# Optimization experiments

Measured on AMD Instinct MI355X. Metric: run time of the kernel, lower is better.

## Reference

```python
import jax, jax.numpy as jnp
import numpy as np

H = 16  # n_heads from init_kwargs


def setup_inputs() -> dict:
    key = jax.random.key(0)
    ks = jax.random.split(key, 9)
    B, N, D = 4, 4096, 1024
    mk = lambda k, shape: jax.random.normal(k, shape, dtype=jnp.float32) * 0.02
    return {
        "x": jax.random.normal(ks[0], (B, N, D), dtype=jnp.float32),
        "Wq": mk(ks[1], (D, D)), "bq": mk(ks[2], (D,)),
        "Wk": mk(ks[3], (D, D)), "bk": mk(ks[4], (D,)),
        "Wv": mk(ks[5], (D, D)), "bv": mk(ks[6], (D,)),
        "Wo": mk(ks[7], (D, D)), "bo": mk(ks[8], (D,)),
    }


def _split_heads(t):
    B, N, D = t.shape
    return t.reshape(B, N, H, D // H).transpose(0, 2, 1, 3)  # b h n d


def reference(x, Wq, bq, Wk, bk, Wv, bv, Wo, bo):
    B, N, D = x.shape
    d_head = D // H
    s = (d_head ** 0.5) ** (-0.25)
    q = _split_heads(x @ Wq + bq)
    # NOTE: original computes key(x) but immediately overwrites it with
    # q.softmax(dim=-2); key projection is dead code. We replicate exactly.
    _ = x @ Wk + bk  # dead, kept for parameter-shape parity
    v = _split_heads(x @ Wv + bv)
    q = jax.nn.softmax(q, axis=-1) * s            # softmax over d_head
    k = jax.nn.softmax(q, axis=-2) * s            # softmax of q over seq dim (faithful!)
    ctx = jnp.einsum('bhnd,bhne->bhde', k, v)     # k^T @ v, [B,H,d,d]
    attn = jnp.einsum('bhnd,bhde->bhne', q, ctx)  # q @ ctx, [B,H,N,d]
    attn = attn.transpose(0, 2, 1, 3).reshape(B, N, D)
    # n_heads > 1 -> to_out linear; dropout is identity in eval mode
    return attn @ Wo + bo
```

## Files before the change

kernel.cpp:

```cpp
#include <hip/hip_runtime.h>

typedef unsigned short u16;
typedef __attribute__((ext_vector_type(8))) short short8;
typedef __attribute__((ext_vector_type(4))) float f4;
typedef __attribute__((ext_vector_type(8))) unsigned short us8;

__device__ __forceinline__ u16 f2bf(float f) {
    unsigned u = __float_as_uint(f);
    u += 0x7FFFu + ((u >> 16) & 1u);
    return (u16)(u >> 16);
}
__device__ __forceinline__ float bf2f(u16 h) {
    return __uint_as_float(((unsigned)h) << 16);
}

#define GLD16(gp, lp) __builtin_amdgcn_global_load_lds( \
    (const __attribute__((address_space(1))) void*)(gp), \
    (__attribute__((address_space(3))) void*)(lp), 16, 0, 0)

#define SCALE_S 0.594603557501360533f

__global__ __launch_bounds__(256) void convert_f32_bf16(const float* __restrict__ in,
                                                        u16* __restrict__ out) {
    const size_t i = (size_t)blockIdx.x * 256 + threadIdx.x;
    const float4* p = (const float4*)in + i * 2;
    float4 a = p[0], b = p[1];
    us8 r;
    r[0] = f2bf(a.x); r[1] = f2bf(a.y); r[2] = f2bf(a.z); r[3] = f2bf(a.w);
    r[4] = f2bf(b.x); r[5] = f2bf(b.y); r[6] = f2bf(b.z); r[7] = f2bf(b.w);
    *(us8*)(out + i * 8) = r;
}

__global__ __launch_bounds__(256) void transpose_convert3(
    const float* __restrict__ Wq, const float* __restrict__ Wv, const float* __restrict__ Wo,
    u16* __restrict__ WqvT, u16* __restrict__ WoT) {
    const float* W; u16* out;
    if (blockIdx.z == 0)      { W = Wq; out = WqvT; }
    else if (blockIdx.z == 1) { W = Wv; out = WqvT + 1024 * 1024; }
    else                      { W = Wo; out = WoT; }
    __shared__ float tile[32][33];
    const int tx = threadIdx.x, ty = threadIdx.y;
    const int x = blockIdx.x * 32 + tx;
#pragma unroll
    for (int i = 0; i < 4; ++i) {
        const int y = blockIdx.y * 32 + ty + i * 8;
        tile[ty + i * 8][tx] = W[(size_t)y * 1024 + x];
    }
    __syncthreads();
#pragma unroll
    for (int i = 0; i < 4; ++i) {
        const int yo = blockIdx.x * 32 + ty + i * 8;
        const int xo = blockIdx.y * 32 + tx;
        out[(size_t)yo * 1024 + xo] = f2bf(tile[tx][ty + i * 8]);
    }
}

__global__ void concat_bias(const float* __restrict__ bq, const float* __restrict__ bv,
                            float* __restrict__ bqv) {
    const int i = blockIdx.x * 256 + threadIdx.x;
    bqv[i] = (i < 1024) ? bq[i] : bv[i - 1024];
}

#define BAR8() do { asm volatile("" ::: "memory"); __builtin_amdgcn_s_barrier(); \
                    asm volatile("" ::: "memory"); } while (0)
#define WAITV(n) asm volatile("s_waitcnt vmcnt(" #n ")" ::: "memory")

#define STG2(arr, p, half) do { \
    const u16* s_ = (p) + (size_t)(half) * 128 * 1024; \
    u16* d_ = &arr[half][ldst]; \
    GLD16(s_, d_); \
    GLD16(s_ + (size_t)64 * 1024, d_ + 64 * 64); \
} while (0)

#define MFMA_CL(base) \
    _Pragma("unroll") for (int kk_ = 0; kk_ < 2; ++kk_) \
    _Pragma("unroll") for (int i_ = 0; i_ < 4; ++i_) \
    _Pragma("unroll") for (int j_ = 0; j_ < 4; ++j_) \
        acc[(base) + i_][j_] = __builtin_amdgcn_mfma_f32_16x16x32_bf16( \
            bf[j_][kk_], af[i_][kk_], acc[(base) + i_][j_], 0, 0, 0);

#define KTILE3(AsR, BsR, AsW, BsW) do { \
    short8 bf[4][2]; \
    _Pragma("unroll") for (int j_ = 0; j_ < 4; ++j_) \
    _Pragma("unroll") for (int kk_ = 0; kk_ < 2; ++kk_) \
        bf[j_][kk_] = *(const short8*)&BsR[bhalf][(brow + j_ * 16 + lrow) * 64 + (kg0 ^ (kk_ << 5))]; \
    { \
        short8 af[4][2]; \
        _Pragma("unroll") for (int i_ = 0; i_ < 4; ++i_) \
        _Pragma("unroll") for (int kk_ = 0; kk_ < 2; ++kk_) \
            af[i_][kk_] = *(const short8*)&AsR[wrow][(i_ * 16 + lrow) * 64 + (kg0 ^ (kk_ << 5))]; \
        STG2(AsW, aP, 0); STG2(AsW, aP, 1); aP += 64; \
        __builtin_amdgcn_s_setprio(1); \
        MFMA_CL(0) \
        __builtin_amdgcn_s_setprio(0); \
    } \
    { \
        short8 af[4][2]; \
        _Pragma("unroll") for (int i_ = 0; i_ < 4; ++i_) \
        _Pragma("unroll") for (int kk_ = 0; kk_ < 2; ++kk_) \
            af[i_][kk_] = *(const short8*)&AsR[wrow][((64 + i_ * 16 + lrow)) * 64 + (kg0 ^ (kk_ << 5))]; \
        BAR8(); \
        STG2(BsW, bP, 0); STG2(BsW, bP, 1); bP += 64; \
        __builtin_amdgcn_s_setprio(1); \
        MFMA_CL(4) \
        __builtin_amdgcn_s_setprio(0); \
    } \
    WAITV(8); \
    BAR8(); \
} while (0)

#define KTILE_NOSYNC(AsR, BsR) do { \
    short8 bf[4][2]; \
    _Pragma("unroll") for (int j_ = 0; j_ < 4; ++j_) \
    _Pragma("unroll") for (int kk_ = 0; kk_ < 2; ++kk_) \
        bf[j_][kk_] = *(const short8*)&BsR[bhalf][(brow + j_ * 16 + lrow) * 64 + (kg0 ^ (kk_ << 5))]; \
    _Pragma("unroll") for (int h_ = 0; h_ < 2; ++h_) { \
        short8 af[4][2]; \
        _Pragma("unroll") for (int i_ = 0; i_ < 4; ++i_) \
        _Pragma("unroll") for (int kk_ = 0; kk_ < 2; ++kk_) \
            af[i_][kk_] = *(const short8*)&AsR[wrow][((h_ * 64 + i_ * 16 + lrow)) * 64 + (kg0 ^ (kk_ << 5))]; \
        if (h_ == 0) { MFMA_CL(0) } else { MFMA_CL(4) } \
    } \
} while (0)

#define GEMM_PRO_AND_LOOP() \
    STG2(Bs0, bS, 0); STG2(Bs0, bS, 1); \
    STG2(As0, aS, 0); STG2(As0, aS, 1); \
    { const u16* b1 = bS + 64; STG2(Bs1, b1, 0); STG2(Bs1, b1, 1); } \
    { const u16* a1 = aS + 64; STG2(As1, a1, 0); STG2(As1, a1, 1); } \
    WAITV(8); \
    BAR8(); \
    const u16* aP = aS + 128; \
    const u16* bP = bS + 128; \
    for (int it6 = 0; it6 < 2; ++it6) { \
        KTILE3(As0, Bs0, As2, Bs0); \
        KTILE3(As1, Bs1, As0, Bs1); \
        KTILE3(As2, Bs0, As1, Bs0); \
        KTILE3(As0, Bs1, As2, Bs1); \
        KTILE3(As1, Bs0, As0, Bs0); \
        KTILE3(As2, Bs1, As1, Bs1); \
    } \
    KTILE3(As0, Bs0, As2, Bs0);   \
    KTILE3(As1, Bs1, As0, Bs1);   \
    WAITV(0); \
    BAR8(); \
    KTILE_NOSYNC(As2, Bs0);       \
    KTILE_NOSYNC(As0, Bs1);

__global__ __launch_bounds__(512, 2) void gemm_qv(
    const u16* __restrict__ A, const u16* __restrict__ BT,
    const float* __restrict__ bias,
    u16* __restrict__ qsOut, u16* __restrict__ vOut)
{
    __shared__ u16 As0[2][128 * 64], As1[2][128 * 64], As2[2][128 * 64];
    __shared__ u16 Bs0[2][128 * 64], Bs1[2][128 * 64];
    const int t = threadIdx.x;
    const int l = t & 63, w = t >> 6;
    const int quad = l >> 4, lrow = l & 15;
    const int wrow = w >> 2, wcol = w & 3;
    const int bhalf = wcol >> 1, brow = (wcol & 1) * 64;

    int bx, by;
    {
        const int id = blockIdx.x + (int)gridDim.x * blockIdx.y;
        const int xcd = id & 7, j = id >> 3;
        const int xs = (int)gridDim.x >> 3;
        bx = xcd * xs + (j % xs);
        by = j / xs;
    }
    const int m0 = bx * 256, n0 = by * 256;

    const int lr0 = t >> 3;
    const int cg = ((t & 7) ^ (lr0 & 7)) * 8;
    const int ldst = lr0 * 64 + (t & 7) * 8;
    const u16* aS = A  + (size_t)(m0 + lr0) * 1024 + cg;
    const u16* bS = BT + (size_t)(n0 + lr0) * 1024 + cg;

    const int kg0 = (quad ^ (lrow & 7)) << 3;
    f4 acc[8][4] = {};

    GEMM_PRO_AND_LOOP()

    const int colh = n0 + wcol * 64;
    const bool isQ = n0 < 1024;
    float4 bs4[4];
#pragma unroll
    for (int j = 0; j < 4; ++j)
        bs4[j] = *(const float4*)&bias[colh + j * 16 + quad * 4];

#pragma unroll
    for (int i = 0; i < 8; ++i) {
        const int m = m0 + wrow * 128 + i * 16 + lrow;
        float v[4][4];
#pragma unroll
        for (int j = 0; j < 4; ++j) {
            v[j][0] = acc[i][j][0] + bs4[j].x;
            v[j][1] = acc[i][j][1] + bs4[j].y;
            v[j][2] = acc[i][j][2] + bs4[j].z;
            v[j][3] = acc[i][j][3] + bs4[j].w;
        }
        if (isQ) {
            float mx = v[0][0];
#pragma unroll
            for (int j = 0; j < 4; ++j)
#pragma unroll
                for (int r = 0; r < 4; ++r) mx = fmaxf(mx, v[j][r]);
            mx = fmaxf(mx, __shfl_xor(mx, 16));
            mx = fmaxf(mx, __shfl_xor(mx, 32));
            float sm = 0.f;
#pragma unroll
            for (int j = 0; j < 4; ++j)
#pragma unroll
                for (int r = 0; r < 4; ++r) { v[j][r] = __expf(v[j][r] - mx); sm += v[j][r]; }
            sm += __shfl_xor(sm, 16);
            sm += __shfl_xor(sm, 32);
            const float inv = SCALE_S / sm;
            u16* qp = qsOut + (size_t)m * 1024 + colh + quad * 4;
#pragma unroll
            for (int j = 0; j < 4; ++j) {
                uint2 pk;
                pk.x = (unsigned)f2bf(v[j][0] * inv) | ((unsigned)f2bf(v[j][1] * inv) << 16);
                pk.y = (unsigned)f2bf(v[j][2] * inv) | ((unsigned)f2bf(v[j][3] * inv) << 16);
                *(uint2*)(qp + j * 16) = pk;
            }
        } else {
            u16* vp = vOut + (size_t)m * 1024 + (colh - 1024) + quad * 4;
#pragma unroll
            for (int j = 0; j < 4; ++j) {
                uint2 pk;
                pk.x = (unsigned)f2bf(v[j][0]) | ((unsigned)f2bf(v[j][1]) << 16);
                pk.y = (unsigned)f2bf(v[j][2]) | ((unsigned)f2bf(v[j][3]) << 16);
                *(uint2*)(vp + j * 16) = pk;
            }
        }
    }
}

__global__ __launch_bounds__(512, 2) void gemm_out(
    const u16* __restrict__ A, const u16* __restrict__ BT,
    const float* __restrict__ bias, float* __restrict__ C)
{
    __shared__ u16 As0[2][128 * 64], As1[2][128 * 64], As2[2][128 * 64];
    __shared__ u16 Bs0[2][128 * 64], Bs1[2][128 * 64];
    const int t = threadIdx.x;
    const int l = t & 63, w = t >> 6;
    const int quad = l >> 4, lrow = l & 15;
    const int wrow = w >> 2, wcol = w & 3;
    const int bhalf = wcol >> 1, brow = (wcol & 1) * 64;
    const int z = blockIdx.z;
    A  += (size_t)z * (4096 * 1024);
    BT += (size_t)z * (1024 * 1024);
    C  += (size_t)z * (4096 * 1024);

    int bx, by;
    {
        const int id = blockIdx.x + (int)gridDim.x * blockIdx.y;
        const int xcd = id & 7, j = id >> 3;
        const int xs = (int)gridDim.x >> 3;
        bx = xcd * xs + (j % xs);
        by = j / xs;
    }
    const int m0 = bx * 256, n0 = by * 256;

    const int lr0 = t >> 3;
    const int cg = ((t & 7) ^ (lr0 & 7)) * 8;
    const int ldst = lr0 * 64 + (t & 7) * 8;
    const u16* aS = A  + (size_t)(m0 + lr0) * 1024 + cg;
    const u16* bS = BT + (size_t)(n0 + lr0) * 1024 + cg;

    const int kg0 = (quad ^ (lrow & 7)) << 3;
    f4 acc[8][4] = {};

    GEMM_PRO_AND_LOOP()

    const int colh = n0 + wcol * 64;
    float4 bs4[4];
#pragma unroll
    for (int j = 0; j < 4; ++j)
        bs4[j] = *(const float4*)&bias[colh + j * 16 + quad * 4];
#pragma unroll
    for (int i = 0; i < 8; ++i) {
        const int m = m0 + wrow * 128 + i * 16 + lrow;
        float* cp = C + (size_t)m * 1024 + colh + quad * 4;
#pragma unroll
        for (int j = 0; j < 4; ++j) {
            float4 o;
            o.x = acc[i][j][0] + bs4[j].x;
            o.y = acc[i][j][1] + bs4[j].y;
            o.z = acc[i][j][2] + bs4[j].z;
            o.w = acc[i][j][3] + bs4[j].w;
            *(float4*)(cp + j * 16) = o;
        }
    }
}

__global__ __launch_bounds__(256) void ctx_mfma(
    const u16* __restrict__ qs, const u16* __restrict__ vb,
    float* __restrict__ Mpart, float* __restrict__ Zpart)
{
    __shared__ __align__(16) u16 Et[2][64 * 64];
    __shared__ __align__(16) u16 Vt[2][64 * 64];
    const int t = threadIdx.x;
    const int w = t >> 6, l = t & 63;
    const int quad = l >> 4, lrow = l & 15;
    const int g = blockIdx.x;
    const int split = blockIdx.y;
    const int b = g >> 4, h = g & 15;

    const int n0 = (l & 31) * 2;
    const int d0 = w * 16 + (l >> 5) * 8;
    const u16* qp = qs + ((size_t)b * 4096 + (size_t)split * 256 + n0) * 1024 + h * 64 + d0;
    const u16* vp = vb + ((size_t)b * 4096 + (size_t)split * 256 + n0) * 1024 + h * 64 + d0;

    f4 acc[4] = {};
    float zacc[8] = {};

    us8 q8a = *(const us8*)qp;
    us8 q8b = *(const us8*)(qp + 1024);
    us8 v8a = *(const us8*)vp;
    us8 v8b = *(const us8*)(vp + 1024);

    for (int slab = 0; slab < 4; ++slab) {
        unsigned epk[8], vpk[8];
#pragma unroll
        for (int j = 0; j < 8; ++j) {
            float ea = __expf(bf2f((u16)q8a[j]));
            float eb = __expf(bf2f((u16)q8b[j]));
            zacc[j] += ea + eb;
            epk[j] = (unsigned)f2bf(ea) | ((unsigned)f2bf(eb) << 16);
            vpk[j] = (unsigned)(u16)v8a[j] | ((unsigned)(u16)v8b[j] << 16);
        }
        if (slab < 3) {
            qp += 64 * 1024; vp += 64 * 1024;
            q8a = *(const us8*)qp;  q8b = *(const us8*)(qp + 1024);
            v8a = *(const us8*)vp;  v8b = *(const us8*)(vp + 1024);
        }
        u16* et = Et[slab & 1];
        u16* vt = Vt[slab & 1];
#pragma unroll
        for (int j = 0; j < 8; ++j) {
            const int d = d0 + j;
            const int off = d * 64 + (((n0 >> 3) ^ (d & 7)) << 3) + (n0 & 7);
            *(unsigned*)&et[off] = epk[j];
            *(unsigned*)&vt[off] = vpk[j];
        }
        __syncthreads();
#pragma unroll
        for (int kk = 0; kk < 2; ++kk) {
            const int blk = ((kk * 4 + quad) ^ (lrow & 7)) << 3;
            short8 a = *(const short8*)&et[(w * 16 + lrow) * 64 + blk];
#pragma unroll
            for (int j = 0; j < 4; ++j) {
                short8 bfr = *(const short8*)&vt[(j * 16 + lrow) * 64 + blk];
                acc[j] = __builtin_amdgcn_mfma_f32_16x16x32_bf16(bfr, a, acc[j], 0, 0, 0);
            }
        }
    }

#pragma unroll
    for (int j = 0; j < 8; ++j) {
        zacc[j] += __shfl_xor(zacc[j], 1);
        zacc[j] += __shfl_xor(zacc[j], 2);
        zacc[j] += __shfl_xor(zacc[j], 4);
        zacc[j] += __shfl_xor(zacc[j], 8);
        zacc[j] += __shfl_xor(zacc[j], 16);
    }
    if ((l & 31) == 0) {
        float* zp = Zpart + ((size_t)split * 64 + g) * 64 + d0;
#pragma unroll
        for (int j = 0; j < 8; ++j) zp[j] = zacc[j];
    }

    float* mp = Mpart + ((size_t)split * 64 + g) * 4096;
#pragma unroll
    for (int j = 0; j < 4; ++j) {
        float4 o;
        o.x = acc[j][0]; o.y = acc[j][1]; o.z = acc[j][2]; o.w = acc[j][3];
        *(float4*)&mp[(w * 16 + lrow) * 64 + j * 16 + quad * 4] = o;
    }
}

__global__ __launch_bounds__(256) void ctx_norm(const float* __restrict__ Mpart,
                                                const float* __restrict__ Zpart,
                                                float* __restrict__ ctx2) {
    const int g = blockIdx.x >> 2, q = blockIdx.x & 3, t = threadIdx.x;
    __shared__ float rz[64];
    if (t < 64) {
        float zsum = 0.f;
#pragma unroll
        for (int s = 0; s < 16; ++s) zsum += Zpart[((size_t)s * 64 + g) * 64 + t];
        rz[t] = SCALE_S / zsum;
    }
    __syncthreads();
    const int base = q * 1024;
    for (int ii = t; ii < 1024; ii += 256) {
        const int idx = base + ii;
        float m = 0.f;
#pragma unroll
        for (int s = 0; s < 16; ++s) m += Mpart[((size_t)s * 64 + g) * 4096 + idx];
        ctx2[(size_t)g * 4096 + idx] = m * rz[idx >> 6];
    }
}

__global__ __launch_bounds__(256) void woprime(const float* __restrict__ ctx2,
                                               const u16* __restrict__ WoT,
                                               u16* __restrict__ WopT) {
    __shared__ float ctxT[64 * 65];
    __shared__ __align__(16) u16 wo[64 * 64];
    const int t = threadIdx.x;
    const int jt = blockIdx.x, h = blockIdx.y, b = blockIdx.z;
    const int g = b * 16 + h;
    for (int idx = t; idx < 4096; idx += 256) {
        const int d = idx >> 6, e = idx & 63;
        ctxT[e * 65 + d] = ctx2[(size_t)g * 4096 + idx];
    }
    const int j0 = jt * 64;
#pragma unroll
    for (int c = 0; c < 2; ++c) {
        const int ii = c * 256 + t;
        const int j = ii >> 3, c8 = ii & 7;
        *(us8*)&wo[j * 64 + c8 * 8] = *(const us8*)&WoT[(size_t)(j0 + j) * 1024 + h * 64 + c8 * 8];
    }
    __syncthreads();
    const int d = t & 63, w = t >> 6;
    float accj[16] = {};
    for (int eb = 0; eb < 8; ++eb) {
        float c8[8];
#pragma unroll
        for (int e = 0; e < 8; ++e) c8[e] = ctxT[(eb * 8 + e) * 65 + d];
#pragma unroll
        for (int jj = 0; jj < 16; ++jj) {
            us8 w8 = *(const us8*)&wo[(jj * 4 + w) * 64 + eb * 8];
#pragma unroll
            for (int e = 0; e < 8; ++e)
                accj[jj] += bf2f((u16)w8[e]) * c8[e];
        }
    }
#pragma unroll
    for (int jj = 0; jj < 16; ++jj)
        WopT[(size_t)b * 1048576 + (size_t)(j0 + jj * 4 + w) * 1024 + h * 64 + d] = f2bf(accj[jj]);
}

extern "C" void kernel_launch(void* const* d_in, const int* in_sizes, int n_in,
                              void* d_out, int out_size, void* d_ws, size_t ws_size,
                              hipStream_t stream)
{
    const float* x  = (const float*)d_in[0];
    const float* Wq = (const float*)d_in[1];
    const float* bq = (const float*)d_in[2];
    const float* Wv = (const float*)d_in[5];
    const float* bv = (const float*)d_in[6];
    const float* Wo = (const float*)d_in[7];
    const float* bo = (const float*)d_in[8];
    float* out = (float*)d_out;

    char* ws = (char*)d_ws;
    size_t o = 0;
    auto alloc = [&](size_t bytes) { char* p = ws + o; o = (o + bytes + 255) & ~(size_t)255; return p; };
    u16*   x_bf  = (u16*)  alloc(16384ull * 1024 * 2);
    u16*   WqvT  = (u16*)  alloc(2048ull * 1024 * 2);
    u16*   WoT   = (u16*)  alloc(1024ull * 1024 * 2);
    float* bqv   = (float*)alloc(2048ull * 4);
    u16*   qs    = (u16*)  alloc(16384ull * 1024 * 2);
    u16*   vbuf  = (u16*)  alloc(16384ull * 1024 * 2);
    float* Zpart = (float*)alloc(16ull * 64 * 64 * 4);
    float* ctx2  = (float*)alloc(64ull * 4096 * 4);
    u16*   WopT  = (u16*)  alloc(4ull * 1024 * 1024 * 2);
    float* Mpart = (float*)x_bf;
    (void)ws_size; (void)in_sizes; (void)n_in; (void)out_size;

    convert_f32_bf16<<<8192, 256, 0, stream>>>(x, x_bf);
    transpose_convert3<<<dim3(32, 32, 3), dim3(32, 8), 0, stream>>>(Wq, Wv, Wo, WqvT, WoT);
    concat_bias<<<8, 256, 0, stream>>>(bq, bv, bqv);

    gemm_qv<<<dim3(64, 8), 512, 0, stream>>>(x_bf, WqvT, bqv, qs, vbuf);
    ctx_mfma<<<dim3(64, 16), 256, 0, stream>>>(qs, vbuf, Mpart, Zpart);
    ctx_norm<<<256, 256, 0, stream>>>(Mpart, Zpart, ctx2);
    woprime<<<dim3(16, 16, 4), 256, 0, stream>>>(ctx2, WoT, WopT);
    gemm_out<<<dim3(16, 4, 4), 512, 0, stream>>>(qs, WopT, bo, out);
}
```

Baseline: 300.2 us.

## Prefetch next B fragments into registers across K-tiles in QV GEMM

Restructures the GEMM main loop so each K-tile reads both A-fragment halves up front and uses B fragments already held in registers (bfc) from the previous iteration. The next tile's B fragments are read from LDS mid-tile, between the two MFMA clusters, which overlaps LDS reads with compute. The vmcnt wait moves earlier and the barrier placement changes. This costs extra VGPRs for the doubled fragment buffers, which could spill or lower occupancy at launch_bounds(512,2).

Result: slower. 307.7 us (+2.5%).

```diff
diff --git a/kernel.cpp b/kernel.cpp
--- a/kernel.cpp
+++ b/kernel.cpp
@@ -72,80 +72,83 @@
     GLD16(s_ + (size_t)64 * 1024, d_ + 64 * 64); \
 } while (0)
 
-#define MFMA_CL(base) \
+#define RD_AF(af, AsR, roff) \
+    _Pragma("unroll") for (int i_ = 0; i_ < 4; ++i_) \
+    _Pragma("unroll") for (int kk_ = 0; kk_ < 2; ++kk_) \
+        af[i_][kk_] = *(const short8*)&AsR[wrow][((roff) + i_ * 16 + lrow) * 64 + (kg0 ^ (kk_ << 5))];
+
+#define RD_BF(bfa, BsX) \
+    _Pragma("unroll") for (int j_ = 0; j_ < 4; ++j_) \
+    _Pragma("unroll") for (int kk_ = 0; kk_ < 2; ++kk_) \
+        bfa[j_][kk_] = *(const short8*)&BsX[bhalf][(brow + j_ * 16 + lrow) * 64 + (kg0 ^ (kk_ << 5))];
+
+#define MFMA_C(base, bfa, afa) \
     _Pragma("unroll") for (int kk_ = 0; kk_ < 2; ++kk_) \
     _Pragma("unroll") for (int i_ = 0; i_ < 4; ++i_) \
     _Pragma("unroll") for (int j_ = 0; j_ < 4; ++j_) \
         acc[(base) + i_][j_] = __builtin_amdgcn_mfma_f32_16x16x32_bf16( \
-            bf[j_][kk_], af[i_][kk_], acc[(base) + i_][j_], 0, 0, 0);
-
-#define KTILE3(AsR, BsR, AsW, BsW) do { \
-    short8 bf[4][2]; \
+            bfa[j_][kk_], afa[i_][kk_], acc[(base) + i_][j_], 0, 0, 0);
+
+#define KTILE_D(AsR, BsN, AsW, BsW) do { \
+    short8 af0[4][2], af1[4][2]; \
+    RD_AF(af0, AsR, 0) \
+    RD_AF(af1, AsR, 64) \
+    STG2(AsW, aP, 0); STG2(AsW, aP, 1); aP += 64; \
+    WAITV(4); \
+    __builtin_amdgcn_s_setprio(1); MFMA_C(0, bfc, af0) __builtin_amdgcn_s_setprio(0); \
+    BAR8(); \
+    short8 bfn[4][2]; \
+    RD_BF(bfn, BsN) \
+    STG2(BsW, bP, 0); STG2(BsW, bP, 1); bP += 64; \
+    __builtin_amdgcn_s_setprio(1); MFMA_C(4, bfc, af1) __builtin_amdgcn_s_setprio(0); \
+    BAR8(); \
     _Pragma("unroll") for (int j_ = 0; j_ < 4; ++j_) \
     _Pragma("unroll") for (int kk_ = 0; kk_ < 2; ++kk_) \
-        bf[j_][kk_] = *(const short8*)&BsR[bhalf][(brow + j_ * 16 + lrow) * 64 + (kg0 ^ (kk_ << 5))]; \
-    { \
-        short8 af[4][2]; \
-        _Pragma("unroll") for (int i_ = 0; i_ < 4; ++i_) \
-        _Pragma("unroll") for (int kk_ = 0; kk_ < 2; ++kk_) \
-            af[i_][kk_] = *(const short8*)&AsR[wrow][(i_ * 16 + lrow) * 64 + (kg0 ^ (kk_ << 5))]; \
-        STG2(AsW, aP, 0); STG2(AsW, aP, 1); aP += 64; \
-        __builtin_amdgcn_s_setprio(1); \
-        MFMA_CL(0) \
-        __builtin_amdgcn_s_setprio(0); \
-    } \
-    { \
-        short8 af[4][2]; \
-        _Pragma("unroll") for (int i_ = 0; i_ < 4; ++i_) \
-        _Pragma("unroll") for (int kk_ = 0; kk_ < 2; ++kk_) \
-            af[i_][kk_] = *(const short8*)&AsR[wrow][((64 + i_ * 16 + lrow)) * 64 + (kg0 ^ (kk_ << 5))]; \
-        BAR8(); \
-        STG2(BsW, bP, 0); STG2(BsW, bP, 1); bP += 64; \
-        __builtin_amdgcn_s_setprio(1); \
-        MFMA_CL(4) \
-        __builtin_amdgcn_s_setprio(0); \
-    } \
+        bfc[j_][kk_] = bfn[j_][kk_]; \
+} while (0)
+
+#define GEMM_PRO_AND_LOOP() \
+    STG2(As0, aS, 0); STG2(As0, aS, 1); \
+    STG2(Bs0, bS, 0); STG2(Bs0, bS, 1); \
+    { const u16* a1 = aS + 64; STG2(As1, a1, 0); STG2(As1, a1, 1); } \
+    { const u16* b1 = bS + 64; STG2(Bs1, b1, 0); STG2(Bs1, b1, 1); } \
     WAITV(8); \
     BAR8(); \
-} while (0)
-
-#define KTILE_NOSYNC(AsR, BsR) do { \
-    short8 bf[4][2]; \
-    _Pragma("unroll") for (int j_ = 0; j_ < 4; ++j_) \
-    _Pragma("unroll") for (int kk_ = 0; kk_ < 2; ++kk_) \
-        bf[j_][kk_] = *(const short8*)&BsR[bhalf][(brow + j_ * 16 + lrow) * 64 + (kg0 ^ (kk_ << 5))]; \
-    _Pragma("unroll") for (int h_ = 0; h_ < 2; ++h_) { \
-        short8 af[4][2]; \
-        _Pragma("unroll") for (int i_ = 0; i_ < 4; ++i_) \
-        _Pragma("unroll") for (int kk_ = 0; kk_ < 2; ++kk_) \
-            af[i_][kk_] = *(const short8*)&AsR[wrow][((h_ * 64 + i_ * 16 + lrow)) * 64 + (kg0 ^ (kk_ << 5))]; \
-        if (h_ == 0) { MFMA_CL(0) } else { MFMA_CL(4) } \
-    } \
-} while (0)
-
-#define GEMM_PRO_AND_LOOP() \
-    STG2(Bs0, bS, 0); STG2(Bs0, bS, 1); \
-    STG2(As0, aS, 0); STG2(As0, aS, 1); \
-    { const u16* b1 = bS + 64; STG2(Bs1, b1, 0); STG2(Bs1, b1, 1); } \
-    { const u16* a1 = aS + 64; STG2(As1, a1, 0); STG2(As1, a1, 1); } \
-    WAITV(8); \
-    BAR8(); \
+    short8 bfc[4][2]; \
+    RD_BF(bfc, Bs0) \
     const u16* aP = aS + 128; \
     const u16* bP = bS + 128; \
-    for (int it6 = 0; it6 < 2; ++it6) { \
-        KTILE3(As0, Bs0, As2, Bs0); \
-        KTILE3(As1, Bs1, As0, Bs1); \
-        KTILE3(As2, Bs0, As1, Bs0); \
-        KTILE3(As0, Bs1, As2, Bs1); \
-        KTILE3(As1, Bs0, As0, Bs0); \
-        KTILE3(As2, Bs1, As1, Bs1); \
+    for (int g6 = 0; g6 < 2; ++g6) { \
+        KTILE_D(As0, Bs1, As2, Bs0);   \
+        KTILE_D(As1, Bs0, As0, Bs1);   \
+        KTILE_D(As2, Bs1, As1, Bs0);   \
+        KTILE_D(As0, Bs0, As2, Bs1);   \
+        KTILE_D(As1, Bs1, As0, Bs0);   \
+        KTILE_D(As2, Bs0, As1, Bs1);   \
     } \
-    KTILE3(As0, Bs0, As2, Bs0);   \
-    KTILE3(As1, Bs1, As0, Bs1);   \
-    WAITV(0); \
-    BAR8(); \
-    KTILE_NOSYNC(As2, Bs0);       \
-    KTILE_NOSYNC(As0, Bs1);
+    KTILE_D(As0, Bs1, As2, Bs0);       \
+    KTILE_D(As1, Bs0, As0, Bs1);       \
+    {    \
+        short8 af0[4][2], af1[4][2]; \
+        RD_AF(af0, As2, 0) \
+        RD_AF(af1, As2, 64) \
+        WAITV(0); \
+        __builtin_amdgcn_s_setprio(1); MFMA_C(0, bfc, af0) __builtin_amdgcn_s_setprio(0); \
+        BAR8(); \
+        short8 bfn[4][2]; \
+        RD_BF(bfn, Bs1) \
+        __builtin_amdgcn_s_setprio(1); MFMA_C(4, bfc, af1) __builtin_amdgcn_s_setprio(0); \
+        _Pragma("unroll") for (int j_ = 0; j_ < 4; ++j_) \
+        _Pragma("unroll") for (int kk_ = 0; kk_ < 2; ++kk_) \
+            bfc[j_][kk_] = bfn[j_][kk_]; \
+    } \
+    {    \
+        short8 af0[4][2], af1[4][2]; \
+        RD_AF(af0, As0, 0) \
+        RD_AF(af1, As0, 64) \
+        MFMA_C(0, bfc, af0) \
+        MFMA_C(4, bfc, af1) \
+    }
 
 __global__ __launch_bounds__(512, 2) void gemm_qv(
     const u16* __restrict__ A, const u16* __restrict__ BT,
```
